# Kernel optimization log

Hardware: AMD Instinct MI355X
Metric: run time of the kernel (lower is better)

## Reference

```python
import jax, jax.numpy as jnp
import numpy as np

B, T, D, H, A = 1024, 128, 64, 256, 8  # batch, seq_len, state_dim, hidden_dim, action_dim


def setup_inputs() -> dict:
    key = jax.random.key(0)
    ks = jax.random.split(key, 12)
    k = 1.0 / np.sqrt(H)  # PyTorch LSTM/Linear default init range
    u = lambda kk, shape: jax.random.uniform(kk, shape, jnp.float32, -k, k)
    return {
        "state": jax.random.normal(ks[0], (B, 1, D), jnp.float32),
        "gamma": jnp.ones((D,), jnp.float32),
        "beta": jnp.zeros((D,), jnp.float32),
        "W_ih0": u(ks[1], (4 * H, D)),
        "W_hh0": u(ks[2], (4 * H, H)),
        "b_ih0": u(ks[3], (4 * H,)),
        "b_hh0": u(ks[4], (4 * H,)),
        "W_ih1": u(ks[5], (4 * H, H)),
        "W_hh1": u(ks[6], (4 * H, H)),
        "b_ih1": u(ks[7], (4 * H,)),
        "b_hh1": u(ks[8], (4 * H,)),
        "fcW": u(ks[9], (A, H)),
        "fcb": u(ks[10], (A,)),
        "seq_len": T,
    }


def _lstm_cell(x, h, c, Wih, Whh, b):
    # PyTorch gate order: input, forget, cell(g), output
    g = x @ Wih.T + h @ Whh.T + b
    i, f, gg, o = jnp.split(g, 4, axis=-1)
    c_new = jax.nn.sigmoid(f) * c + jax.nn.sigmoid(i) * jnp.tanh(gg)
    h_new = jax.nn.sigmoid(o) * jnp.tanh(c_new)
    return h_new, c_new


def reference(state, gamma, beta, W_ih0, W_hh0, b_ih0, b_hh0,
              W_ih1, W_hh1, b_ih1, b_hh1, fcW, fcb, seq_len):
    # state: [B, 1, D]; the same (layernormed) input is fed every timestep,
    # only the LSTM hidden/cell state evolves.
    x = state[:, 0, :]  # [B, D]
    mu = x.mean(-1, keepdims=True)
    var = ((x - mu) ** 2).mean(-1, keepdims=True)
    xn = (x - mu) * jax.lax.rsqrt(var + 1e-5) * gamma + beta  # LayerNorm(state_dim)

    b0 = b_ih0 + b_hh0
    b1 = b_ih1 + b_hh1
    bsz = x.shape[0]
    hdim = W_hh0.shape[1]
    z = jnp.zeros((bsz, hdim), x.dtype)
    init = (z, z, z, z)  # (h0, c0, h1, c1); h=None -> zeros in torch

    def step(carry, _):
        h0, c0, h1, c1 = carry
        h0, c0 = _lstm_cell(xn, h0, c0, W_ih0, W_hh0, b0)  # layer 0
        h1, c1 = _lstm_cell(h0, h1, c1, W_ih1, W_hh1, b1)  # layer 1
        action = jnp.tanh(h1 @ fcW.T + fcb)  # [B, A]
        return (h0, c0, h1, c1), action

    _, actions = jax.lax.scan(step, init, None, length=seq_len)  # [T, B, A]
    return jnp.transpose(actions, (1, 0, 2))  # [B, T, A]
```

## Files before the change

### kernel.cpp

```cpp
#include <hip/hip_runtime.h>
#include <math.h>

#define B_    1024
#define T_    128
#define D_    64
#define H_    256
#define A_    8

#define NG    8
#define NB    32
#define MB    128
#define SL    8
#define FSTR  32

typedef __attribute__((ext_vector_type(8))) short short8;
typedef __attribute__((ext_vector_type(4))) float floatx4;

__device__ __forceinline__ short f2bf(float f) {
    union { float f; unsigned u; } x; x.f = f;
    return (short)((x.u + 0x7FFFu + ((x.u >> 16) & 1u)) >> 16);
}
__device__ __forceinline__ float bf2f(short s) {
    union { unsigned u; float f; } x;
    x.u = ((unsigned)(unsigned short)s) << 16;
    return x.f;
}
__device__ __forceinline__ float sigm(float x) {
    return __builtin_amdgcn_rcpf(1.0f + __expf(-x));
}
__device__ __forceinline__ float ftanh(float x) {
    float t = __expf(-2.0f * fabsf(x));
    float r = (1.0f - t) * __builtin_amdgcn_rcpf(1.0f + t);
    return copysignf(r, x);
}

__device__ __forceinline__ void cell_update(floatx4 aA, floatx4 aB, float* cpair,
                                            short* __restrict__ Hw, size_t rowbase,
                                            int colbase, int hi, int rsel) {
    floatx4 tA, tB;
#pragma unroll
    for (int r = 0; r < 4; ++r) {
        tA[r] = __shfl_xor(aA[r], 8, 64);
        tB[r] = __shfl_xor(aB[r], 8, 64);
    }
#pragma unroll
    for (int rr = 0; rr < 2; ++rr) {
        int r = rsel + rr;
        float gi = hi ? tA[r] : aA[r];
        float gf = hi ? aA[r] : tA[r];
        float gg = hi ? tB[r] : aB[r];
        float go = hi ? aB[r] : tB[r];
        float cn = sigm(gf) * cpair[rr] + sigm(gi) * ftanh(gg);
        float hn = sigm(go) * ftanh(cn);
        cpair[rr] = cn;
        Hw[(rowbase + r) * H_ + colbase] = f2bf(hn);
    }
}

__global__ void __launch_bounds__(512)
actor_kernel(const float* __restrict__ state, const float* __restrict__ gamma,
             const float* __restrict__ beta,  const float* __restrict__ Wih0,
             const float* __restrict__ Whh0,  const float* __restrict__ bih0,
             const float* __restrict__ bhh0,  const float* __restrict__ Wih1,
             const float* __restrict__ Whh1,  const float* __restrict__ bih1,
             const float* __restrict__ bhh1,  const float* __restrict__ fcW,
             const float* __restrict__ fcb,   float* __restrict__ out,
             unsigned* __restrict__ flags, unsigned* __restrict__ aux,
             short* __restrict__ Hb0, short* __restrict__ Hb1)
{
    __shared__ __attribute__((aligned(16))) short sWp[24576];
    __shared__ int sMap[3];

    const int blk  = blockIdx.x;
    const int tid  = threadIdx.x;
    const int lane = tid & 63;
    const int wave = tid >> 6;

    if (tid == 0) {
        unsigned xcc;
        asm volatile("s_getreg_b32 %0, hwreg(HW_REG_XCC_ID)" : "=s"(xcc));
        xcc &= 7u;
        unsigned r = atomicAdd(&aux[xcc * 16], 1u);
        __hip_atomic_fetch_add(&aux[256], 1u, __ATOMIC_ACQ_REL,
                               __HIP_MEMORY_SCOPE_AGENT);
        while (__hip_atomic_load(&aux[256], __ATOMIC_RELAXED,
                                 __HIP_MEMORY_SCOPE_AGENT) < (unsigned)gridDim.x)
            __builtin_amdgcn_s_sleep(1);
        __builtin_amdgcn_fence(__ATOMIC_ACQUIRE, "agent");
        int pre = 0, tot = 0; bool ok = true;
        for (int x = 0; x < 8; ++x) {
            int cx = (int)__hip_atomic_load(&aux[x * 16], __ATOMIC_RELAXED,
                                            __HIP_MEMORY_SCOPE_AGENT);
            if (cx & 31) ok = false;
            if (x < (int)xcc) pre += cx >> 5;
            tot += cx >> 5;
        }
        if (tot != NG) ok = false;
        sMap[0] = ok ? (pre + (int)(r >> 5)) : (blk & 7);
        sMap[1] = ok ? (int)(r & 31)         : (blk >> 3);
        sMap[2] = ok ? 1 : 0;
    }
    __syncthreads();
    const int  g     = sMap[0];
    const int  s     = sMap[1];
    const bool fastp = (sMap[2] != 0);
    const int  g128  = g * MB;

    const int q4   = lane >> 4;
    const int l15  = lane & 15;
    const int jj   = l15 & 7;
    const int hi   = l15 >> 3;
    const int rg0  = hi * H_ + s * SL + jj;
    const int rg1  = (2 + hi) * H_ + s * SL + jj;
    const int mrow = wave * 16 + q4 * 4;
    const int colbase = s * SL + jj;
    const int rsel = hi * 2;

    float* sXn = (float*)sWp;
    if (tid < MB) {
        const float* xr = state + (size_t)(g128 + tid) * D_;
        float mu = 0.f;
        for (int d = 0; d < D_; ++d) mu += xr[d];
        mu *= (1.0f / D_);
        float var = 0.f;
        for (int d = 0; d < D_; ++d) { float t = xr[d] - mu; var += t * t; }
        var *= (1.0f / D_);
        float is = rsqrtf(var + 1e-5f);
        for (int d = 0; d < D_; ++d)
            sXn[tid * 65 + d] = (xr[d] - mu) * is * gamma[d] + beta[d];
    }
    __syncthreads();

    const float b0v0 = bih0[rg0] + bhh0[rg0];
    const float b0v1 = bih0[rg1] + bhh0[rg1];
    const float b1v0 = bih1[rg0] + bhh1[rg0];
    const float b1v1 = bih1[rg1] + bhh1[rg1];

    floatx4 pre0a, pre0b;
    {
        const float* w0 = Wih0 + (size_t)rg0 * D_;
        const float* w1 = Wih0 + (size_t)rg1 * D_;
#pragma unroll
        for (int r = 0; r < 4; ++r) { pre0a[r] = b0v0; pre0b[r] = b0v1; }
        for (int d = 0; d < D_; ++d) {
            float wa = w0[d], wb = w1[d];
#pragma unroll
            for (int r = 0; r < 4; ++r) {
                float xv = sXn[(mrow + r) * 65 + d];
                pre0a[r] += xv * wa;
                pre0b[r] += xv * wb;
            }
        }
    }
    __syncthreads();

    const int fo = lane >> 3, fk8 = lane & 7;
    float fcw_r[32];
#pragma unroll
    for (int kk = 0; kk < 32; ++kk) fcw_r[kk] = fcW[fo * H_ + fk8 * 32 + kk];
    const float fcb_r = fcb[fo];

    for (int idx = tid; idx < 8192; idx += 512) {
        int kt = idx >> 10, rem = idx & 1023;
        int c = rem >> 9, rem2 = rem & 511;
        int ln = rem2 >> 3, j = rem2 & 7;
        int q4_ = ln >> 4, l15_ = ln & 15;
        int n = c * 16 + l15_;
        int r = (n >> 3) * H_ + s * SL + (n & 7);
        int k = kt * 32 + q4_ * 8 + j;
        sWp[idx] = f2bf(Whh0[(size_t)r * H_ + k]);
    }
    for (int idx = tid; idx < 16384; idx += 512) {
        int kt = idx >> 11, rem = idx & 2047;
        int c = rem >> 9, rem2 = rem & 511;
        int ln = rem2 >> 3, j = rem2 & 7;
        int q4_ = ln >> 4, l15_ = ln & 15;
        int n = (c & 1) * 16 + l15_;
        int r = (n >> 3) * H_ + s * SL + (n & 7);
        int k = kt * 32 + q4_ * 8 + j;
        float v = (c >> 1) ? Whh1[(size_t)r * H_ + k] : Wih1[(size_t)r * H_ + k];
        sWp[8192 + idx] = f2bf(v);
    }
    float c0[2] = {0.f, 0.f}, c1[2] = {0.f, 0.f};
    __syncthreads();

    short8 bw0[16];
#pragma unroll
    for (int kt = 0; kt < 8; ++kt) {
        bw0[2 * kt]     = *(const short8*)(sWp + kt * 1024 + lane * 8);
        bw0[2 * kt + 1] = *(const short8*)(sWp + kt * 1024 + 512 + lane * 8);
    }
    const short* ldsB = sWp + 8192 + lane * 8;

    const int BH = B_ * H_;
    for (int ph = 0; ph <= T_ + 1; ++ph) {
        const short* H0r  = Hb0 + ((ph + 1) & 1) * BH;
        short*       H0w  = Hb0 + (ph & 1) * BH;
        const short* H1r2 = Hb1 + (ph & 1) * BH;
        short*       H1w  = Hb1 + ((ph + 1) & 1) * BH;

        const bool doL0 = (ph < T_);
        const bool doL1 = (ph >= 1 && ph <= T_);

        if (ph >= 2 && wave < 4) {
            int t = ph - 2;
            int b = 4 * s + wave;
            const short8* hp = (const short8*)(H1r2 + (size_t)(g128 + b) * H_ + fk8 * 32);
            float sum = 0.f;
#pragma unroll
            for (int c8 = 0; c8 < 4; ++c8) {
                short8 hv = hp[c8];
#pragma unroll
                for (int j = 0; j < 8; ++j)
                    sum += bf2f(hv[j]) * fcw_r[c8 * 8 + j];
            }
            sum += __shfl_down(sum, 4, 8);
            sum += __shfl_down(sum, 2, 8);
            sum += __shfl_down(sum, 1, 8);
            if (fk8 == 0)
                out[((size_t)(g128 + b) * T_ + t) * A_ + fo] = ftanh(sum + fcb_r);
        }

        if (doL0 || doL1) {
            short8 a0[8], a1[8];
            const short* ap = H0r + (size_t)(g128 + wave * 16 + l15) * H_ + q4 * 8;
#pragma unroll
            for (int kt = 0; kt < 8; ++kt)
                a0[kt] = *(const short8*)(ap + kt * 32);
            if (doL1) {
                const short* cp = H1r2 + (size_t)(g128 + wave * 16 + l15) * H_ + q4 * 8;
#pragma unroll
                for (int kt = 0; kt < 8; ++kt)
                    a1[kt] = *(const short8*)(cp + kt * 32);
            }

            floatx4 l0a = pre0a, l0b = pre0b, l1a, l1b;
#pragma unroll
            for (int r = 0; r < 4; ++r) { l1a[r] = b1v0; l1b[r] = b1v1; }

#pragma unroll
            for (int kt = 0; kt < 8; ++kt) {
                if (doL0) {
                    l0a = __builtin_amdgcn_mfma_f32_16x16x32_bf16(a0[kt], bw0[2 * kt],     l0a, 0, 0, 0);
                    l0b = __builtin_amdgcn_mfma_f32_16x16x32_bf16(a0[kt], bw0[2 * kt + 1], l0b, 0, 0, 0);
                }
                if (doL1) {
                    short8 bia = *(const short8*)(ldsB + kt * 2048);
                    short8 bib = *(const short8*)(ldsB + kt * 2048 + 512);
                    short8 bha = *(const short8*)(ldsB + kt * 2048 + 1024);
                    short8 bhb = *(const short8*)(ldsB + kt * 2048 + 1536);
                    l1a = __builtin_amdgcn_mfma_f32_16x16x32_bf16(a0[kt], bia, l1a, 0, 0, 0);
                    l1b = __builtin_amdgcn_mfma_f32_16x16x32_bf16(a0[kt], bib, l1b, 0, 0, 0);
                    l1a = __builtin_amdgcn_mfma_f32_16x16x32_bf16(a1[kt], bha, l1a, 0, 0, 0);
                    l1b = __builtin_amdgcn_mfma_f32_16x16x32_bf16(a1[kt], bhb, l1b, 0, 0, 0);
                }
            }

            size_t rowbase = (size_t)(g128 + mrow);
            if (doL0) cell_update(l0a, l0b, c0, H0w, rowbase, colbase, hi, rsel);
            if (doL1) cell_update(l1a, l1b, c1, H1w, rowbase, colbase, hi, rsel);
        }

        if (ph <= T_) {
            __syncthreads();
            const unsigned val = (unsigned)(ph + 2);
            if (tid == 0) {
                if (!fastp) __builtin_amdgcn_fence(__ATOMIC_RELEASE, "agent");
                __hip_atomic_store(&flags[(g * NB + s) * FSTR], val,
                                   __ATOMIC_RELAXED, __HIP_MEMORY_SCOPE_AGENT);
            }
            if (wave == 7 && lane < NB) {
                while (__hip_atomic_load(&flags[(g * NB + lane) * FSTR],
                                         __ATOMIC_RELAXED, __HIP_MEMORY_SCOPE_AGENT)
                       < val)
                    __builtin_amdgcn_s_sleep(1);
            }
            __syncthreads();
            if (fastp) { asm volatile("buffer_inv sc0" ::: "memory"); }
            else       { __builtin_amdgcn_fence(__ATOMIC_ACQUIRE, "agent"); }
        }
    }
}

extern "C" void kernel_launch(void* const* d_in, const int* in_sizes, int n_in,
                              void* d_out, int out_size, void* d_ws, size_t ws_size,
                              hipStream_t stream)
{
    const float* state = (const float*)d_in[0];
    const float* gamma = (const float*)d_in[1];
    const float* beta  = (const float*)d_in[2];
    const float* Wih0  = (const float*)d_in[3];
    const float* Whh0  = (const float*)d_in[4];
    const float* bih0  = (const float*)d_in[5];
    const float* bhh0  = (const float*)d_in[6];
    const float* Wih1  = (const float*)d_in[7];
    const float* Whh1  = (const float*)d_in[8];
    const float* bih1  = (const float*)d_in[9];
    const float* bhh1  = (const float*)d_in[10];
    const float* fcW   = (const float*)d_in[11];
    const float* fcb   = (const float*)d_in[12];
    float* out = (float*)d_out;

    unsigned* flags = (unsigned*)d_ws;
    unsigned* aux   = (unsigned*)((char*)d_ws + 32768);
    short* Hb0 = (short*)((char*)d_ws + 36864);
    short* Hb1 = Hb0 + 2 * B_ * H_;

    size_t zbytes = 36864 + (size_t)4 * B_ * H_ * sizeof(short);
    hipMemsetAsync(d_ws, 0, zbytes, stream);

    void* args[] = { &state, &gamma, &beta, &Wih0, &Whh0, &bih0, &bhh0,
                     &Wih1, &Whh1, &bih1, &bhh1, &fcW, &fcb, &out,
                     &flags, &aux, &Hb0, &Hb1 };
    hipError_t err = hipLaunchCooperativeKernel((const void*)actor_kernel,
                                                dim3(NG * NB), dim3(512),
                                                args, 0, stream);
    if (err != hipSuccess) {
        (void)hipGetLastError();
        actor_kernel<<<dim3(NG * NB), dim3(512), 0, stream>>>(
            state, gamma, beta, Wih0, Whh0, bih0, bhh0,
            Wih1, Whh1, bih1, bhh1, fcW, fcb, out, flags, aux, Hb0, Hb1);
    }
    (void)in_sizes; (void)n_in; (void)out_size; (void)ws_size;
}
```

Measured before the change: 961.6 us.

## Halve block to 256 threads with each wave processing two row tiles

The block shrinks from 8 to 4 waves, and each wave now loops over two 64-row halves of the block's 128 batch rows. The layer-0 recurrent weights are read from LDS every step instead of staying in registers, which frees registers for the doubled per-wave state. The aim is cheaper block barriers and flag spinning per timestep. The cost is twice the serial MFMA and cell-update work per wave on the critical recurrent path, plus extra LDS traffic.

```diff
diff --git a/kernel.cpp b/kernel.cpp
--- a/kernel.cpp
+++ b/kernel.cpp
@@ -57,7 +57,7 @@
     }
 }
 
-__global__ void __launch_bounds__(512)
+__global__ void __launch_bounds__(256)
 actor_kernel(const float* __restrict__ state, const float* __restrict__ gamma,
              const float* __restrict__ beta,  const float* __restrict__ Wih0,
              const float* __restrict__ Whh0,  const float* __restrict__ bih0,
@@ -68,7 +68,7 @@
              unsigned* __restrict__ flags, unsigned* __restrict__ aux,
              short* __restrict__ Hb0, short* __restrict__ Hb1)
 {
-    __shared__ __attribute__((aligned(16))) short sWp[24576];
+    __shared__ __attribute__((aligned(16))) short sWp[28672];
     __shared__ int sMap[3];
 
     const int blk  = blockIdx.x;
@@ -136,20 +136,24 @@
     const float b1v0 = bih1[rg0] + bhh1[rg0];
     const float b1v1 = bih1[rg1] + bhh1[rg1];
 
-    floatx4 pre0a, pre0b;
+    floatx4 pre0a[2], pre0b[2];
     {
         const float* w0 = Wih0 + (size_t)rg0 * D_;
         const float* w1 = Wih0 + (size_t)rg1 * D_;
 #pragma unroll
-        for (int r = 0; r < 4; ++r) { pre0a[r] = b0v0; pre0b[r] = b0v1; }
+        for (int u = 0; u < 2; ++u)
+#pragma unroll
+            for (int r = 0; r < 4; ++r) { pre0a[u][r] = b0v0; pre0b[u][r] = b0v1; }
         for (int d = 0; d < D_; ++d) {
             float wa = w0[d], wb = w1[d];
 #pragma unroll
-            for (int r = 0; r < 4; ++r) {
-                float xv = sXn[(mrow + r) * 65 + d];
-                pre0a[r] += xv * wa;
-                pre0b[r] += xv * wb;
-            }
+            for (int u = 0; u < 2; ++u)
+#pragma unroll
+                for (int r = 0; r < 4; ++r) {
+                    float xv = sXn[(u * 64 + mrow + r) * 65 + d];
+                    pre0a[u][r] += xv * wa;
+                    pre0b[u][r] += xv * wb;
+                }
         }
     }
     __syncthreads();
@@ -160,7 +164,7 @@
     for (int kk = 0; kk < 32; ++kk) fcw_r[kk] = fcW[fo * H_ + fk8 * 32 + kk];
     const float fcb_r = fcb[fo];
 
-    for (int idx = tid; idx < 8192; idx += 512) {
+    for (int idx = tid; idx < 8192; idx += 256) {
         int kt = idx >> 10, rem = idx & 1023;
         int c = rem >> 9, rem2 = rem & 511;
         int ln = rem2 >> 3, j = rem2 & 7;
@@ -170,7 +174,7 @@
         int k = kt * 32 + q4_ * 8 + j;
         sWp[idx] = f2bf(Whh0[(size_t)r * H_ + k]);
     }
-    for (int idx = tid; idx < 16384; idx += 512) {
+    for (int idx = tid; idx < 16384; idx += 256) {
         int kt = idx >> 11, rem = idx & 2047;
         int c = rem >> 9, rem2 = rem & 511;
         int ln = rem2 >> 3, j = rem2 & 7;
@@ -181,16 +185,11 @@
         float v = (c >> 1) ? Whh1[(size_t)r * H_ + k] : Wih1[(size_t)r * H_ + k];
         sWp[8192 + idx] = f2bf(v);
     }
-    float c0[2] = {0.f, 0.f}, c1[2] = {0.f, 0.f};
+    float c0[2][2] = {{0.f,0.f},{0.f,0.f}}, c1[2][2] = {{0.f,0.f},{0.f,0.f}};
     __syncthreads();
 
-    short8 bw0[16];
-#pragma unroll
-    for (int kt = 0; kt < 8; ++kt) {
-        bw0[2 * kt]     = *(const short8*)(sWp + kt * 1024 + lane * 8);
-        bw0[2 * kt + 1] = *(const short8*)(sWp + kt * 1024 + 512 + lane * 8);
-    }
-    const short* ldsB = sWp + 8192 + lane * 8;
+    const short* ldsB0 = sWp + lane * 8;
+    const short* ldsB1 = sWp + 8192 + lane * 8;
 
     const int BH = B_ * H_;
     for (int ph = 0; ph <= T_ + 1; ++ph) {
@@ -202,7 +201,7 @@
         const bool doL0 = (ph < T_);
         const bool doL1 = (ph >= 1 && ph <= T_);
 
-        if (ph >= 2 && wave < 4) {
+        if (ph >= 2) {
             int t = ph - 2;
             int b = 4 * s + wave;
             const short8* hp = (const short8*)(H1r2 + (size_t)(g128 + b) * H_ + fk8 * 32);
@@ -222,43 +221,49 @@
         }
 
         if (doL0 || doL1) {
-            short8 a0[8], a1[8];
-            const short* ap = H0r + (size_t)(g128 + wave * 16 + l15) * H_ + q4 * 8;
-#pragma unroll
-            for (int kt = 0; kt < 8; ++kt)
-                a0[kt] = *(const short8*)(ap + kt * 32);
-            if (doL1) {
-                const short* cp = H1r2 + (size_t)(g128 + wave * 16 + l15) * H_ + q4 * 8;
+#pragma unroll
+            for (int u = 0; u < 2; ++u) {
+                short8 a0[8], a1[8];
+                const size_t arow = (size_t)(g128 + u * 64 + wave * 16 + l15) * H_ + q4 * 8;
+                const short* ap = H0r + arow;
 #pragma unroll
                 for (int kt = 0; kt < 8; ++kt)
-                    a1[kt] = *(const short8*)(cp + kt * 32);
+                    a0[kt] = *(const short8*)(ap + kt * 32);
+                if (doL1) {
+                    const short* cp = H1r2 + arow;
+#pragma unroll
+                    for (int kt = 0; kt < 8; ++kt)
+                        a1[kt] = *(const short8*)(cp + kt * 32);
+                }
+
+                floatx4 l0a = pre0a[u], l0b = pre0b[u], l1a, l1b;
+#pragma unroll
+                for (int r = 0; r < 4; ++r) { l1a[r] = b1v0; l1b[r] = b1v1; }
+
+#pragma unroll
+                for (int kt = 0; kt < 8; ++kt) {
+                    if (doL0) {
+                        short8 b0a = *(const short8*)(ldsB0 + kt * 1024);
+                        short8 b0b = *(const short8*)(ldsB0 + kt * 1024 + 512);
+                        l0a = __builtin_amdgcn_mfma_f32_16x16x32_bf16(a0[kt], b0a, l0a, 0, 0, 0);
+                        l0b = __builtin_amdgcn_mfma_f32_16x16x32_bf16(a0[kt], b0b, l0b, 0, 0, 0);
+                    }
+                    if (doL1) {
+                        short8 bia = *(const short8*)(ldsB1 + kt * 2048);
+                        short8 bib = *(const short8*)(ldsB1 + kt * 2048 + 512);
+                        short8 bha = *(const short8*)(ldsB1 + kt * 2048 + 1024);
+                        short8 bhb = *(const short8*)(ldsB1 + kt * 2048 + 1536);
+                        l1a = __builtin_amdgcn_mfma_f32_16x16x32_bf16(a0[kt], bia, l1a, 0, 0, 0);
+                        l1b = __builtin_amdgcn_mfma_f32_16x16x32_bf16(a0[kt], bib, l1b, 0, 0, 0);
+                        l1a = __builtin_amdgcn_mfma_f32_16x16x32_bf16(a1[kt], bha, l1a, 0, 0, 0);
+                        l1b = __builtin_amdgcn_mfma_f32_16x16x32_bf16(a1[kt], bhb, l1b, 0, 0, 0);
+                    }
+                }
+
+                size_t rowbase = (size_t)(g128 + u * 64 + mrow);
+                if (doL0) cell_update(l0a, l0b, c0[u], H0w, rowbase, colbase, hi, rsel);
+                if (doL1) cell_update(l1a, l1b, c1[u], H1w, rowbase, colbase, hi, rsel);
             }
-
-            floatx4 l0a = pre0a, l0b = pre0b, l1a, l1b;
-#pragma unroll
-            for (int r = 0; r < 4; ++r) { l1a[r] = b1v0; l1b[r] = b1v1; }
-
-#pragma unroll
-            for (int kt = 0; kt < 8; ++kt) {
-                if (doL0) {
-                    l0a = __builtin_amdgcn_mfma_f32_16x16x32_bf16(a0[kt], bw0[2 * kt],     l0a, 0, 0, 0);
-                    l0b = __builtin_amdgcn_mfma_f32_16x16x32_bf16(a0[kt], bw0[2 * kt + 1], l0b, 0, 0, 0);
-                }
-                if (doL1) {
-                    short8 bia = *(const short8*)(ldsB + kt * 2048);
-                    short8 bib = *(const short8*)(ldsB + kt * 2048 + 512);
-                    short8 bha = *(const short8*)(ldsB + kt * 2048 + 1024);
-                    short8 bhb = *(const short8*)(ldsB + kt * 2048 + 1536);
-                    l1a = __builtin_amdgcn_mfma_f32_16x16x32_bf16(a0[kt], bia, l1a, 0, 0, 0);
-                    l1b = __builtin_amdgcn_mfma_f32_16x16x32_bf16(a0[kt], bib, l1b, 0, 0, 0);
-                    l1a = __builtin_amdgcn_mfma_f32_16x16x32_bf16(a1[kt], bha, l1a, 0, 0, 0);
-                    l1b = __builtin_amdgcn_mfma_f32_16x16x32_bf16(a1[kt], bhb, l1b, 0, 0, 0);
-                }
-            }
-
-            size_t rowbase = (size_t)(g128 + mrow);
-            if (doL0) cell_update(l0a, l0b, c0, H0w, rowbase, colbase, hi, rsel);
-            if (doL1) cell_update(l1a, l1b, c1, H1w, rowbase, colbase, hi, rsel);
         }
 
         if (ph <= T_) {
@@ -269,7 +274,7 @@
                 __hip_atomic_store(&flags[(g * NB + s) * FSTR], val,
                                    __ATOMIC_RELAXED, __HIP_MEMORY_SCOPE_AGENT);
             }
-            if (wave == 7 && lane < NB) {
+            if (wave == 0 && lane < NB) {
                 while (__hip_atomic_load(&flags[(g * NB + lane) * FSTR],
                                          __ATOMIC_RELAXED, __HIP_MEMORY_SCOPE_AGENT)
                        < val)
@@ -313,11 +318,11 @@
                      &Wih1, &Whh1, &bih1, &bhh1, &fcW, &fcb, &out,
                      &flags, &aux, &Hb0, &Hb1 };
     hipError_t err = hipLaunchCooperativeKernel((const void*)actor_kernel,
-                                                dim3(NG * NB), dim3(512),
+                                                dim3(NG * NB), dim3(256),
                                                 args, 0, stream);
     if (err != hipSuccess) {
         (void)hipGetLastError();
-        actor_kernel<<<dim3(NG * NB), dim3(512), 0, stream>>>(
+        actor_kernel<<<dim3(NG * NB), dim3(256), 0, stream>>>(
             state, gamma, beta, Wih0, Whh0, bih0, bhh0,
             Wih1, Whh1, bih1, bhh1, fcW, fcb, out, flags, aux, Hb0, Hb1);
     }
```

Result: slower. 1.095 ms (+13.8%).
